# Kernel tuning notes

Hardware: AMD Instinct MI355X
Metric: run time of the kernel (lower is better)

The kernel has to match this reference:

```python
import jax, jax.numpy as jnp
import numpy as np

CLIP_LIMIT = 4.0
N_BINS = 64
GRID = (8, 8, 8)
BANDWIDTH = 0.001


def bspline5(x):
    # Quintic B-spline basis (Thevenaz), support |x| < 3
    t = jnp.abs(x)
    t2 = t * t
    t3 = t2 * t
    t4 = t2 * t2
    t5 = t4 * t
    w0 = 11.0 / 20.0 - t2 / 2.0 + t4 / 4.0 - t5 / 12.0
    w1 = 17.0 / 40.0 + 5.0 * t / 8.0 - 7.0 * t2 / 4.0 + 5.0 * t3 / 4.0 - 3.0 * t4 / 8.0 + t5 / 24.0
    w2 = (3.0 - t) ** 5 / 120.0
    return jnp.where(t < 1.0, w0, jnp.where(t < 2.0, w1, jnp.where(t < 3.0, w2, 0.0)))


def reflect_dct2(i, n):
    # 'reflect' (dct2 / symmetric) boundary: period 2n, mirror including edge
    i = jnp.remainder(i, 2 * n)
    return jnp.where(i < n, i, 2 * n - 1 - i)


def axis_matrix(size, g):
    # Dense [size, g] matrix folding 6-tap quintic spline weights + reflect boundary
    c = jnp.linspace(-0.5 - 0.25 / g, g - 1 + 0.5 + 0.25 / g, size)
    base = jnp.floor(c).astype(jnp.int32) - 2
    taps = base[:, None] + jnp.arange(6)[None, :]            # [size, 6]
    w = bspline5(c[:, None] - taps.astype(c.dtype))          # [size, 6]
    idx = reflect_dct2(taps, g)
    M = jnp.zeros((size, g), dtype=c.dtype)
    return M.at[jnp.arange(size)[:, None], idx].add(w)


def clahe3d(x):
    B, C, D, H, W = x.shape
    gd, gh, gw = GRID
    td, th, tw = D // gd, H // gh, W // gw                   # dims divisible -> no padding
    vpt = td * th * tw
    nt = gd * gh * gw

    # --- per-tile Gaussian-KDE histogram (detached in the original: no_grad pad) ---
    xs = jax.lax.stop_gradient(x)
    tiles = xs.reshape(B * C, gd, td, gh, th, gw, tw)
    tiles = tiles.transpose(0, 1, 3, 5, 2, 4, 6).reshape(B * C, nt, vpt)
    bins = jnp.linspace(0.0, 1.0, N_BINS)
    wk = jnp.exp(-0.5 * ((tiles[..., None] - bins) / BANDWIDTH) ** 2)  # [BC, nt, vpt, nb]
    pdf = wk.mean(axis=-2)
    pdf = pdf / (pdf.sum(-1, keepdims=True) + 1e-10)

    # --- clip + redistribute ---
    histos = (pdf * vpt).reshape(-1, N_BINS)
    limit = max(float(np.floor(CLIP_LIMIT * vpt / N_BINS)), 1.0)
    histos = jnp.minimum(histos, limit)
    clipped = vpt - histos.sum(-1)
    residual = jnp.remainder(clipped, float(N_BINS))
    redist = (clipped - residual) / N_BINS
    histos = histos + redist[:, None] + (jnp.arange(N_BINS)[None, :] < residual[:, None]).astype(histos.dtype)

    # --- CDF per tile ---
    cdf = jnp.cumsum(histos, axis=-1) * (N_BINS - 1) / vpt
    cdf = cdf.reshape(B * C, gd, gh, gw, N_BINS).transpose(0, 4, 1, 2, 3)  # [BC, nb, gd, gh, gw]

    # --- separable quintic spline interpolation over the 3 spatial grid axes ---
    Md, Mh, Mw = axis_matrix(D, gd), axis_matrix(H, gh), axis_matrix(W, gw)
    S = jnp.einsum('bnijk,wk->bnijw', cdf, Mw)
    S = jnp.einsum('bnijw,hj->bnihw', S, Mh)
    S = jnp.einsum('bnihw,di->bdhwn', S, Md)                 # [BC, D, H, W, nb]

    # --- spline interpolation along the bin axis at coordinate x*(nb-1) ---
    cb = x.reshape(B * C, D, H, W) * (N_BINS - 1.0)
    base = jnp.floor(cb).astype(jnp.int32) - 2
    taps = base[..., None] + jnp.arange(6)                   # [BC, D, H, W, 6]
    wb = bspline5(cb[..., None] - taps.astype(cb.dtype))
    idx = reflect_dct2(taps, N_BINS)
    vals = jnp.take_along_axis(S, idx, axis=-1)
    out = (vals * wb).sum(-1).reshape(B, C, D, H, W)

    return (out - out.min()) / (out.max() - out.min() + 1e-10)


def setup_inputs() -> dict:
    key = jax.random.key(0)
    x = jax.random.uniform(key, (1, 1, 128, 128, 128), dtype=jnp.float32)
    return {"x": x}


def reference(x):
    return clahe3d(x)
```

## Files before the change

kernel.cpp:

```cpp
#include <hip/hip_runtime.h>
#include <hip/hip_fp16.h>
#include <math.h>


#define WS_M    0
#define WS_CDF  1024
#define WS_T1D  (1024 + 32768)
#define WS_BMM  (1024 + 32768 + 524288)
#define WS_OH   (WS_BMM + 8192)
#define WS_NEED_HALF_BYTES ((size_t)(WS_OH + 1048576) * 4)

__device__ __forceinline__ float bspline5(float x) {
    float t = fabsf(x);
    float t2 = t * t, t3 = t2 * t, t4 = t2 * t2, t5 = t4 * t;
    float w0 = 11.0f/20.0f - t2*0.5f + t4*0.25f - t5*(1.0f/12.0f);
    float w1 = 17.0f/40.0f + t*(5.0f/8.0f) - t2*(7.0f/4.0f) + t3*(5.0f/4.0f)
             - t4*(3.0f/8.0f) + t5*(1.0f/24.0f);
    float u = 3.0f - t;
    float w2 = u*u*u*u*u*(1.0f/120.0f);
    return t < 1.0f ? w0 : (t < 2.0f ? w1 : (t < 3.0f ? w2 : 0.0f));
}

__device__ __forceinline__ void quintic_w(float u, float wb[6]) {
    float u2 = u*u, u4 = u2*u2, u5 = u4*u;
    float v = 1.0f - u;
    float v2 = v*v, v4 = v2*v2, v5 = v4*v;
    wb[0] = v5 * (1.0f/120.0f);
    wb[5] = u5 * (1.0f/120.0f);
    {
        float t = u + 1.0f;
        float t2 = t*t, t3 = t2*t, t4 = t2*t2, t5 = t4*t;
        wb[1] = 17.0f/40.0f + t*(5.0f/8.0f) - t2*(7.0f/4.0f) + t3*(5.0f/4.0f)
              - t4*(3.0f/8.0f) + t5*(1.0f/24.0f);
    }
    {
        float t = 2.0f - u;
        float t2 = t*t, t3 = t2*t, t4 = t2*t2, t5 = t4*t;
        wb[4] = 17.0f/40.0f + t*(5.0f/8.0f) - t2*(7.0f/4.0f) + t3*(5.0f/4.0f)
              - t4*(3.0f/8.0f) + t5*(1.0f/24.0f);
    }
    wb[2] = 11.0f/20.0f - u2*0.5f + u4*0.25f - u5*(1.0f/12.0f);
    wb[3] = 11.0f/20.0f - v2*0.5f + v4*0.25f - v5*(1.0f/12.0f);
}

__device__ __forceinline__ int reflect16(int t) {
    int r = t & 15;
    return r < 8 ? r : 15 - r;
}

__global__ __launch_bounds__(256) void k1_hist(const float* __restrict__ x,
                                               float* __restrict__ cdfbuf,
                                               float* __restrict__ M) {
    __shared__ float hist[256];
    __shared__ float Ml[1024];
    int t = threadIdx.x;
    int b = blockIdx.x;
    hist[t] = 0.0f;
    if (b == 0) {
        #pragma unroll
        for (int i = 0; i < 4; ++i) Ml[i * 256 + t] = 0.0f;
        __syncthreads();
        if (t < 128) {
            const float step = 8.0625f / 127.0f;
            float c = -0.53125f + (float)t * step;
            int base = (int)floorf(c) - 2;
            #pragma unroll
            for (int tt = 0; tt < 6; ++tt) {
                int tap = base + tt;
                Ml[t * 8 + reflect16(tap)] += bspline5(c - (float)tap);
            }
        }
        __syncthreads();
        #pragma unroll
        for (int i = 0; i < 4; ++i) M[i * 256 + t] = Ml[i * 256 + t];
    }
    __syncthreads();

    int ti = b >> 6, tj = (b >> 3) & 7, tk = b & 7;
    int wv = t >> 6;
    const float inv63 = 1.0f / 63.0f;
    int gbase4 = (((ti * 16) * 128 + tj * 16) * 128 + tk * 16) >> 2;
    const float4* x4 = (const float4*)x;
    #pragma unroll
    for (int itv = 0; itv < 4; ++itv) {
        int vi = itv * 256 + t;
        int c4 = vi & 3, bb = (vi >> 2) & 15, a = vi >> 6;
        float4 v4 = x4[gbase4 + a * 4096 + bb * 32 + c4];
        float vals[4] = {v4.x, v4.y, v4.z, v4.w};
        #pragma unroll
        for (int m = 0; m < 4; ++m) {
            float val = vals[m];
            int b0 = (int)floorf(val * 63.0f + 0.5f);
            float q = (val - (float)b0 * inv63) * 1000.0f;
            float q2 = q * q;
            if (q2 <= 36.0f)
                atomicAdd(&hist[wv * 64 + b0], __expf(-0.5f * q2));
        }
    }
    __syncthreads();

    if (t < 64) {
        float pdf = (hist[t] + hist[64 + t] + hist[128 + t] + hist[192 + t])
                    * (1.0f / 4096.0f);
        float s = pdf;
        #pragma unroll
        for (int off = 32; off >= 1; off >>= 1) s += __shfl_xor(s, off, 64);
        float pdfn = pdf / (s + 1e-10f);
        float histo = fminf(pdfn * 4096.0f, 256.0f);
        float s2 = histo;
        #pragma unroll
        for (int off = 32; off >= 1; off >>= 1) s2 += __shfl_xor(s2, off, 64);
        float clipped = 4096.0f - s2;
        float residual = clipped - floorf(clipped * (1.0f / 64.0f)) * 64.0f;
        float redist = (clipped - residual) * (1.0f / 64.0f);
        float h2 = histo + redist + (((float)t < residual) ? 1.0f : 0.0f);
        float cum = h2;
        #pragma unroll
        for (int off = 1; off < 64; off <<= 1) {
            float p = __shfl_up(cum, off, 64);
            if (t >= off) cum += p;
        }
        cdfbuf[b * 64 + t] = cum * (63.0f / 4096.0f);
    }
}

__global__ __launch_bounds__(256) void k2_t1d(const float* __restrict__ cdfbuf,
                                              const float* __restrict__ M,
                                              float* __restrict__ T1d) {
    int i4 = blockIdx.x * 256 + threadIdx.x;
    int d = i4 >> 10;
    int o4 = i4 & 1023;
    const float4* c4 = (const float4*)cdfbuf;
    float md[8];
    #pragma unroll
    for (int i = 0; i < 8; ++i) md[i] = M[d * 8 + i];
    float4 s = make_float4(0.f, 0.f, 0.f, 0.f);
    #pragma unroll
    for (int i = 0; i < 8; ++i) {
        float4 c = c4[i * 1024 + o4];
        s.x += c.x * md[i]; s.y += c.y * md[i];
        s.z += c.z * md[i]; s.w += c.w * md[i];
    }
    ((float4*)T1d)[i4] = s;
}

template <bool HOUT>
__global__ __launch_bounds__(128) void k3_final(const float* __restrict__ x,
                                                const float* __restrict__ T1d,
                                                const float* __restrict__ M,
                                                float* __restrict__ out,
                                                __half* __restrict__ oh,
                                                float* __restrict__ bmm) {
    __shared__ __half2 t2h[4][256];
    __shared__ float smn[2], smx[2];
    const int lt = threadIdx.x;
    const int b = blockIdx.x;
    const int d = b >> 5;

    const int p = lt >> 5, m = lt & 31;

    const float2* T2 = (const float2*)(T1d + d * 4096);
    float2 cv[16];
    #pragma unroll
    for (int j = 0; j < 8; ++j) {
        cv[2 * j]     = T2[(j * 8 + 2 * p) * 32 + m];
        cv[2 * j + 1] = T2[(j * 8 + 2 * p + 1) * 32 + m];
    }

    const int row0 = b * 4;
    float vs[4];
    #pragma unroll
    for (int it = 0; it < 4; ++it) vs[it] = x[(row0 + it) * 128 + lt];

    float mw[8];
    #pragma unroll
    for (int k = 0; k < 8; ++k) mw[k] = M[lt * 8 + k];
    __half2 mwh[4];
    #pragma unroll
    for (int pp = 0; pp < 4; ++pp) mwh[pp] = __floats2half2_rn(mw[2 * pp], mw[2 * pp + 1]);

    #pragma unroll
    for (int it = 0; it < 4; ++it) {
        int h = (row0 + it) & 127;
        float mh[8];
        #pragma unroll
        for (int j = 0; j < 8; ++j) mh[j] = M[h * 8 + j];
        float2 sk0 = make_float2(0.f, 0.f), sk1 = make_float2(0.f, 0.f);
        #pragma unroll
        for (int j = 0; j < 8; ++j) {
            float mj = mh[j];
            sk0.x += cv[2 * j].x * mj;     sk0.y += cv[2 * j].y * mj;
            sk1.x += cv[2 * j + 1].x * mj; sk1.y += cv[2 * j + 1].y * mj;
        }
        __half2 hn0 = __floats2half2_rn(sk0.x, sk1.x);
        __half2 hn1 = __floats2half2_rn(sk0.y, sk1.y);
        __half2* dst = &t2h[it][p * 64 + 2 * m];
        dst[0] = hn0;
        dst[1] = hn1;
    }
    __syncthreads();

    float mn = 3.4e38f, mx = -3.4e38f;
    #pragma unroll
    for (int it = 0; it < 4; ++it) {
        float v = vs[it];
        float cb = v * 63.0f;
        float fl = floorf(cb);
        int basei = (int)fl - 2;
        float wb[6];
        quintic_w(cb - fl, wb);
        const __half2* t2l = t2h[it];
        float acc = 0.0f;
        #pragma unroll
        for (int tt = 0; tt < 6; ++tt) {
            int tap = basei + tt;
            int r = tap & 127;
            int n = r < 64 ? r : 127 - r;
            __half2 a0 = t2l[n];
            __half2 a1 = t2l[n + 64];
            __half2 a2 = t2l[n + 128];
            __half2 a3 = t2l[n + 192];
            __half2 s2 = __hmul2(a0, mwh[0]);
            s2 = __hfma2(a1, mwh[1], s2);
            s2 = __hfma2(a2, mwh[2], s2);
            s2 = __hfma2(a3, mwh[3], s2);
            float s = __low2float(s2) + __high2float(s2);
            acc += wb[tt] * s;
        }
        if (HOUT) {
            __half ha = __float2half_rn(acc);
            float va = __half2float(ha);
            oh[(row0 + it) * 128 + lt] = ha;
            mn = fminf(mn, va);
            mx = fmaxf(mx, va);
        } else {
            out[(row0 + it) * 128 + lt] = acc;
            mn = fminf(mn, acc);
            mx = fmaxf(mx, acc);
        }
    }

    #pragma unroll
    for (int off = 32; off >= 1; off >>= 1) {
        mn = fminf(mn, __shfl_xor(mn, off, 64));
        mx = fmaxf(mx, __shfl_xor(mx, off, 64));
    }
    int lane = lt & 63, wv = lt >> 6;
    if (lane == 0) { smn[wv] = mn; smx[wv] = mx; }
    __syncthreads();
    if (lt == 0) {
        ((float2*)bmm)[b] = make_float2(fminf(smn[0], smn[1]),
                                        fmaxf(smx[0], smx[1]));
    }
}

template <bool HIN>
__global__ __launch_bounds__(1024) void k4_norm(float* __restrict__ out,
                                                const __half* __restrict__ oh,
                                                const float* __restrict__ bmm) {
    __shared__ float smn[16], smx[16], bc[2];
    int t = threadIdx.x;
    const float4* bm4 = (const float4*)bmm;
    float mn = 3.4e38f, mx = -3.4e38f;
    #pragma unroll
    for (int i = 0; i < 2; ++i) {
        float4 r = bm4[i * 1024 + t];
        mn = fminf(mn, fminf(r.x, r.z));
        mx = fmaxf(mx, fmaxf(r.y, r.w));
    }
    #pragma unroll
    for (int off = 32; off >= 1; off >>= 1) {
        mn = fminf(mn, __shfl_xor(mn, off, 64));
        mx = fmaxf(mx, __shfl_xor(mx, off, 64));
    }
    int lane = t & 63, wv = t >> 6;
    if (lane == 0) { smn[wv] = mn; smx[wv] = mx; }
    __syncthreads();
    if (t == 0) {
        float a = smn[0], b = smx[0];
        #pragma unroll
        for (int i = 1; i < 16; ++i) {
            a = fminf(a, smn[i]);
            b = fmaxf(b, smx[i]);
        }
        bc[0] = a; bc[1] = b;
    }
    __syncthreads();
    float m0 = bc[0];
    float sc = 1.0f / (bc[1] - m0 + 1e-10f);
    int idx = blockIdx.x * 1024 + t;
    float4 val;
    if (HIN) {
        const __half2* oh2 = (const __half2*)oh;
        __half2 a = oh2[2 * idx], b2 = oh2[2 * idx + 1];
        val = make_float4(__low2float(a), __high2float(a),
                          __low2float(b2), __high2float(b2));
    } else {
        val = ((const float4*)out)[idx];
    }
    val.x = (val.x - m0) * sc;
    val.y = (val.y - m0) * sc;
    val.z = (val.z - m0) * sc;
    val.w = (val.w - m0) * sc;
    ((float4*)out)[idx] = val;
}

extern "C" void kernel_launch(void* const* d_in, const int* in_sizes, int n_in,
                              void* d_out, int out_size, void* d_ws, size_t ws_size,
                              hipStream_t stream) {
    const float* x = (const float*)d_in[0];
    float* out = (float*)d_out;
    float* ws = (float*)d_ws;
    float* M      = ws + WS_M;
    float* cdfbuf = ws + WS_CDF;
    float* T1d    = ws + WS_T1D;
    float* bmmp   = ws + WS_BMM;
    __half* oh    = (__half*)(ws + WS_OH);
    const bool use_half = ws_size >= WS_NEED_HALF_BYTES;

    hipLaunchKernelGGL(k1_hist, dim3(512), dim3(256), 0, stream, x, cdfbuf, M);
    hipLaunchKernelGGL(k2_t1d,  dim3(512), dim3(256), 0, stream, cdfbuf, M, T1d);
    if (use_half) {
        hipLaunchKernelGGL((k3_final<true>),  dim3(4096), dim3(128),  0, stream,
                           x, T1d, M, out, oh, bmmp);
        hipLaunchKernelGGL((k4_norm<true>),   dim3(512),  dim3(1024), 0, stream,
                           out, oh, bmmp);
    } else {
        hipLaunchKernelGGL((k3_final<false>), dim3(4096), dim3(128),  0, stream,
                           x, T1d, M, out, oh, bmmp);
        hipLaunchKernelGGL((k4_norm<false>),  dim3(512),  dim3(1024), 0, stream,
                           out, oh, bmmp);
    }
}
```

Baseline: 36.55 us.

## Restructure H-contraction to half2 FMAs and pack bin rows for vector LDS reads

Each thread now loads one bin's 64 column values, converts them to half2, and computes two rows of the H-axis contraction with packed half FMAs instead of fp32. Results go to shared memory as one 16-byte record per bin (4 half2 over the W grid), padded every 8 entries to avoid bank conflicts. The tap loop then does a single float4 LDS read per tap instead of four scalar reads. This cuts LDS instruction count and ALU work, at the cost of fp16 accumulation error and more registers for the 32 half2 columns.

After: 39.36 us. 1.08x slower.

```diff
diff --git a/kernel.cpp b/kernel.cpp
--- a/kernel.cpp
+++ b/kernel.cpp
@@ -151,23 +151,23 @@
                                                 float* __restrict__ out,
                                                 __half* __restrict__ oh,
                                                 float* __restrict__ bmm) {
-    __shared__ __half2 t2h[4][256];
+    __shared__ __align__(16) __half2 t2r[4][288];
     __shared__ float smn[2], smx[2];
     const int lt = threadIdx.x;
     const int b = blockIdx.x;
     const int d = b >> 5;
-
-    const int p = lt >> 5, m = lt & 31;
-
-    const float2* T2 = (const float2*)(T1d + d * 4096);
-    float2 cv[16];
-    #pragma unroll
-    for (int j = 0; j < 8; ++j) {
-        cv[2 * j]     = T2[(j * 8 + 2 * p) * 32 + m];
-        cv[2 * j + 1] = T2[(j * 8 + 2 * p + 1) * 32 + m];
-    }
-
+    const int n = lt & 63, g = lt >> 6;
     const int row0 = b * 4;
+
+    const float* basep = T1d + d * 4096 + n;
+    __half2 colH[32];
+    #pragma unroll
+    for (int jc = 0; jc < 32; ++jc) {
+        float f0 = basep[(2 * jc) * 64];
+        float f1 = basep[(2 * jc + 1) * 64];
+        colH[jc] = __floats2half2_rn(f0, f1);
+    }
+
     float vs[4];
     #pragma unroll
     for (int it = 0; it < 4; ++it) vs[it] = x[(row0 + it) * 128 + lt];
@@ -177,26 +177,28 @@
     for (int k = 0; k < 8; ++k) mw[k] = M[lt * 8 + k];
     __half2 mwh[4];
     #pragma unroll
-    for (int pp = 0; pp < 4; ++pp) mwh[pp] = __floats2half2_rn(mw[2 * pp], mw[2 * pp + 1]);
-
-    #pragma unroll
-    for (int it = 0; it < 4; ++it) {
-        int h = (row0 + it) & 127;
-        float mh[8];
-        #pragma unroll
-        for (int j = 0; j < 8; ++j) mh[j] = M[h * 8 + j];
-        float2 sk0 = make_float2(0.f, 0.f), sk1 = make_float2(0.f, 0.f);
+    for (int c = 0; c < 4; ++c) mwh[c] = __floats2half2_rn(mw[2 * c], mw[2 * c + 1]);
+
+    #pragma unroll
+    for (int rr = 0; rr < 2; ++rr) {
+        int r = 2 * g + rr;
+        int h = (row0 + r) & 127;
+        __half2 acc[4];
+        #pragma unroll
+        for (int c = 0; c < 4; ++c) acc[c] = __floats2half2_rn(0.f, 0.f);
         #pragma unroll
         for (int j = 0; j < 8; ++j) {
-            float mj = mh[j];
-            sk0.x += cv[2 * j].x * mj;     sk0.y += cv[2 * j].y * mj;
-            sk1.x += cv[2 * j + 1].x * mj; sk1.y += cv[2 * j + 1].y * mj;
-        }
-        __half2 hn0 = __floats2half2_rn(sk0.x, sk1.x);
-        __half2 hn1 = __floats2half2_rn(sk0.y, sk1.y);
-        __half2* dst = &t2h[it][p * 64 + 2 * m];
-        dst[0] = hn0;
-        dst[1] = hn1;
+            __half2 mj2 = __half2half2(__float2half_rn(M[h * 8 + j]));
+            #pragma unroll
+            for (int c = 0; c < 4; ++c)
+                acc[c] = __hfma2(colH[j * 4 + c], mj2, acc[c]);
+        }
+        float4 wv4;
+        ((__half2*)&wv4)[0] = acc[0];
+        ((__half2*)&wv4)[1] = acc[1];
+        ((__half2*)&wv4)[2] = acc[2];
+        ((__half2*)&wv4)[3] = acc[3];
+        *(float4*)&t2r[r][4 * (n + (n >> 3))] = wv4;
     }
     __syncthreads();
 
@@ -209,21 +211,21 @@
         int basei = (int)fl - 2;
         float wb[6];
         quintic_w(cb - fl, wb);
-        const __half2* t2l = t2h[it];
         float acc = 0.0f;
         #pragma unroll
         for (int tt = 0; tt < 6; ++tt) {
             int tap = basei + tt;
-            int r = tap & 127;
-            int n = r < 64 ? r : 127 - r;
-            __half2 a0 = t2l[n];
-            __half2 a1 = t2l[n + 64];
-            __half2 a2 = t2l[n + 128];
-            __half2 a3 = t2l[n + 192];
-            __half2 s2 = __hmul2(a0, mwh[0]);
-            s2 = __hfma2(a1, mwh[1], s2);
-            s2 = __hfma2(a2, mwh[2], s2);
-            s2 = __hfma2(a3, mwh[3], s2);
+            int r2 = tap & 127;
+            int nt = r2 < 64 ? r2 : 127 - r2;
+            float4 rv = *(const float4*)&t2r[it][4 * (nt + (nt >> 3))];
+            __half2 h0 = ((__half2*)&rv)[0];
+            __half2 h1 = ((__half2*)&rv)[1];
+            __half2 h2 = ((__half2*)&rv)[2];
+            __half2 h3 = ((__half2*)&rv)[3];
+            __half2 s2 = __hmul2(h0, mwh[0]);
+            s2 = __hfma2(h1, mwh[1], s2);
+            s2 = __hfma2(h2, mwh[2], s2);
+            s2 = __hfma2(h3, mwh[3], s2);
             float s = __low2float(s2) + __high2float(s2);
             acc += wb[tt] * s;
         }
```
